# Performance work log

Measured on AMD Instinct MI355X. Metric: run time of the kernel, lower is better.

The kernel has to match this reference:

```python
import jax, jax.numpy as jnp
import numpy as np

N, E, H, C, HC = 16384, 262144, 4, 128, 512
G, IN, ED, OUT, NCLS = 8, 5, 2, 256, 12
EPS = 1e-5


def _gatv2(x, src, dst, ea, Wl, Wr, We, att, b):
    # GATv2Conv (PyG): score = att . leaky_relu(lin_l(x_j) + lin_r(x_i) + lin_e(e))
    xl = (x @ Wl).reshape(-1, H, C)          # source transform [N,H,C]
    xr = (x @ Wr).reshape(-1, H, C)          # target transform [N,H,C]
    ee = (ea @ We).reshape(-1, H, C)         # edge embedding   [E,H,C]
    s = jax.nn.leaky_relu(xl[src] + xr[dst] + ee, 0.2)
    logit = jnp.einsum('ehc,hc->eh', s, att)            # [E,H]
    m = jax.ops.segment_max(logit, dst, num_segments=N)  # per-dst max
    a = jnp.exp(logit - m[dst])
    denom = jax.ops.segment_sum(a, dst, num_segments=N)
    alpha = a / (denom[dst] + 1e-16)                     # segment softmax
    out = jax.ops.segment_sum(xl[src] * alpha[:, :, None], dst, num_segments=N)
    return out.reshape(-1, HC) + b


def _bn(x, g, b):  # BatchNorm1d, training-mode batch stats
    mu = x.mean(0)
    var = x.var(0)
    return g * (x - mu) * jax.lax.rsqrt(var + EPS) + b


def setup_inputs() -> dict:
    key = jax.random.key(0)
    ks = iter(jax.random.split(key, 32))
    d = {}
    d['x'] = jax.random.normal(next(ks), (N, IN), jnp.float32)
    d['edge_attr'] = jax.random.normal(next(ks), (E, ED), jnp.float32)
    d['edge_index'] = jax.random.randint(next(ks), (2, E), 0, N)
    d['batch'] = jnp.sort(jax.random.randint(next(ks), (N,), 0, G))
    for i, din in zip((1, 2, 3), (IN, HC, HC)):
        d[f'c{i}_Wl'] = jax.random.normal(next(ks), (din, HC), jnp.float32) * 0.05
        d[f'c{i}_Wr'] = jax.random.normal(next(ks), (din, HC), jnp.float32) * 0.05
        d[f'c{i}_We'] = jax.random.normal(next(ks), (ED, HC), jnp.float32) * 0.05
        d[f'c{i}_att'] = jax.random.normal(next(ks), (H, C), jnp.float32) * 0.05
        d[f'c{i}_b'] = jnp.zeros((HC,), jnp.float32)
        d[f'bn{i}_g'] = jnp.ones((HC,), jnp.float32)
        d[f'bn{i}_b'] = jnp.zeros((HC,), jnp.float32)
    d['ge_W1'] = jax.random.normal(next(ks), (HC, OUT), jnp.float32) * 0.05
    d['ge_b1'] = jnp.zeros((OUT,), jnp.float32)
    d['ge_W2'] = jax.random.normal(next(ks), (OUT, OUT), jnp.float32) * 0.05
    d['ge_b2'] = jnp.zeros((OUT,), jnp.float32)
    d['cls_W'] = jax.random.normal(next(ks), (OUT, NCLS), jnp.float32) * 0.05
    d['cls_b'] = jnp.zeros((NCLS,), jnp.float32)
    return d


def reference(x, edge_attr, edge_index, batch,
              c1_Wl, c1_Wr, c1_We, c1_att, c1_b, bn1_g, bn1_b,
              c2_Wl, c2_Wr, c2_We, c2_att, c2_b, bn2_g, bn2_b,
              c3_Wl, c3_Wr, c3_We, c3_att, c3_b, bn3_g, bn3_b,
              ge_W1, ge_b1, ge_W2, ge_b2, cls_W, cls_b):
    src, dst = edge_index[0], edge_index[1]
    x1 = jax.nn.elu(_bn(_gatv2(x, src, dst, edge_attr, c1_Wl, c1_Wr, c1_We, c1_att, c1_b), bn1_g, bn1_b))
    x2 = jax.nn.elu(_bn(_gatv2(x1, src, dst, edge_attr, c2_Wl, c2_Wr, c2_We, c2_att, c2_b), bn2_g, bn2_b)) + x1
    x3 = jax.nn.elu(_bn(_gatv2(x2, src, dst, edge_attr, c3_Wl, c3_Wr, c3_We, c3_att, c3_b), bn3_g, bn3_b)) + x2
    cnt = jax.ops.segment_sum(jnp.ones((N,), x3.dtype), batch, num_segments=G)
    x_pool = jax.ops.segment_sum(x3, batch, num_segments=G) / cnt[:, None]
    emb = jax.nn.relu(x_pool @ ge_W1 + ge_b1) @ ge_W2 + ge_b2
    logits = emb @ cls_W + cls_b
    return logits, emb
```

## Files before the change

kernel.cpp:

```cpp
#include <hip/hip_runtime.h>
#include <math.h>

#define NN    16384
#define NE    262144
#define NHEAD 4
#define HC    512
#define NG    8

typedef __bf16 bf16x8 __attribute__((ext_vector_type(8)));
typedef float floatx4 __attribute__((ext_vector_type(4)));
typedef float f32x2 __attribute__((ext_vector_type(2)));

__device__ __forceinline__ f32x2 sp2(float s) { return (f32x2){s, s}; }
__device__ __forceinline__ f32x2 pkmax(f32x2 a, f32x2 b) {
    f32x2 r; r.x = fmaxf(a.x, b.x); r.y = fmaxf(a.y, b.y); return r;
}

__device__ __forceinline__ unsigned short f2bf(float f) {
    union { float f; unsigned u; } v{f};
    unsigned r = v.u + 0x7FFFu + ((v.u >> 16) & 1u);
    return (unsigned short)(r >> 16);
}
__device__ __forceinline__ float bf2f(unsigned short b) {
    return __uint_as_float((unsigned)b << 16);
}

__device__ __forceinline__ void unpk8v(uint4 v, f32x2* f) {
    f[0] = (f32x2){__uint_as_float(v.x << 16), __uint_as_float(v.x & 0xFFFF0000u)};
    f[1] = (f32x2){__uint_as_float(v.y << 16), __uint_as_float(v.y & 0xFFFF0000u)};
    f[2] = (f32x2){__uint_as_float(v.z << 16), __uint_as_float(v.z & 0xFFFF0000u)};
    f[3] = (f32x2){__uint_as_float(v.w << 16), __uint_as_float(v.w & 0xFFFF0000u)};
}

#define GLD16(g, l) __builtin_amdgcn_global_load_lds( \
    (const __attribute__((address_space(1))) void*)(g), \
    (__attribute__((address_space(3))) void*)(l), 16, 0, 0)

__global__ __launch_bounds__(1024) void k_scan(const int* __restrict__ cnt,
                                               int* __restrict__ rp,
                                               int* __restrict__ offp,
                                               const int* __restrict__ batch,
                                               int* __restrict__ gcnt) {
    __shared__ int part[1024];
    int t = threadIdx.x;
    if (t < NG) {
        int lb[2];
#pragma unroll
        for (int q = 0; q < 2; q++) {
            int target = t + q;
            int lo = 0, hi = NN;
            while (lo < hi) {
                int mid = (lo + hi) >> 1;
                if (batch[mid] < target) lo = mid + 1; else hi = mid;
            }
            lb[q] = lo;
        }
        gcnt[t] = lb[1] - lb[0];
    }
    int base = t * 16;
    int loc[16];
    int s = 0;
#pragma unroll
    for (int i = 0; i < 16; i++) { loc[i] = s; s += cnt[base + i]; }
    part[t] = s;
    __syncthreads();
    for (int off = 1; off < 1024; off <<= 1) {
        int v = 0;
        if (t >= off) v = part[t - off];
        __syncthreads();
        if (t >= off) part[t] += v;
        __syncthreads();
    }
    int excl = (t == 0) ? 0 : part[t - 1];
#pragma unroll
    for (int i = 0; i < 16; i++) {
        int r = excl + loc[i];
        rp[base + i] = r;
        offp[base + i] = r;
    }
    if (t == 1023) rp[NN] = excl + s;
}

__global__ void k_fill(const int* __restrict__ dst, const int* __restrict__ src,
                       const float* __restrict__ ea, int* __restrict__ offp,
                       int* __restrict__ csrc, float2* __restrict__ ce) {
    int e = blockIdx.x * 256 + threadIdx.x;
    if (e < NE) {
        int d = dst[e];
        int pos = atomicAdd(&offp[d], 1);
        csrc[pos] = src[e];
        ce[pos] = *(const float2*)(ea + 2 * (size_t)e);
    }
}

__global__ __launch_bounds__(256) void k_pre(
        const int* __restrict__ dst, int* __restrict__ cnt,
        const float* __restrict__ W0, const float* __restrict__ W1,
        const float* __restrict__ W2, const float* __restrict__ W3,
        unsigned short* __restrict__ Wt2, unsigned short* __restrict__ Wt3,
        const float* __restrict__ x, const float* __restrict__ Wl,
        const float* __restrict__ Wr,
        unsigned short* __restrict__ xl, unsigned short* __restrict__ xr) {
    __shared__ float tile[64][65];
    int bid = blockIdx.x;
    int t = threadIdx.x;
    if (bid >= 1280) {
        int n = (bid - 1280) * 4 + (t >> 6);
        int lane = t & 63;
        int j0 = lane << 3;
        float xs[5];
#pragma unroll
        for (int k = 0; k < 5; k++) xs[k] = x[n * 5 + k];
        float al[8] = {}, ar[8] = {};
#pragma unroll
        for (int k = 0; k < 5; k++) {
            float4 wl0 = *(const float4*)(Wl + k * 512 + j0);
            float4 wl1 = *(const float4*)(Wl + k * 512 + j0 + 4);
            float4 wr0 = *(const float4*)(Wr + k * 512 + j0);
            float4 wr1 = *(const float4*)(Wr + k * 512 + j0 + 4);
            al[0] += xs[k] * wl0.x; al[1] += xs[k] * wl0.y; al[2] += xs[k] * wl0.z; al[3] += xs[k] * wl0.w;
            al[4] += xs[k] * wl1.x; al[5] += xs[k] * wl1.y; al[6] += xs[k] * wl1.z; al[7] += xs[k] * wl1.w;
            ar[0] += xs[k] * wr0.x; ar[1] += xs[k] * wr0.y; ar[2] += xs[k] * wr0.z; ar[3] += xs[k] * wr0.w;
            ar[4] += xs[k] * wr1.x; ar[5] += xs[k] * wr1.y; ar[6] += xs[k] * wr1.z; ar[7] += xs[k] * wr1.w;
        }
        ushort4 o0, o1;
        o0.x = f2bf(al[0]); o0.y = f2bf(al[1]); o0.z = f2bf(al[2]); o0.w = f2bf(al[3]);
        o1.x = f2bf(al[4]); o1.y = f2bf(al[5]); o1.z = f2bf(al[6]); o1.w = f2bf(al[7]);
        *(ushort4*)(xl + (size_t)n * 512 + j0) = o0;
        *(ushort4*)(xl + (size_t)n * 512 + j0 + 4) = o1;
        o0.x = f2bf(ar[0]); o0.y = f2bf(ar[1]); o0.z = f2bf(ar[2]); o0.w = f2bf(ar[3]);
        o1.x = f2bf(ar[4]); o1.y = f2bf(ar[5]); o1.z = f2bf(ar[6]); o1.w = f2bf(ar[7]);
        *(ushort4*)(xr + (size_t)n * 512 + j0) = o0;
        *(ushort4*)(xr + (size_t)n * 512 + j0 + 4) = o1;
    } else if (bid >= 1024) {
        int wb = bid - 1024;
        int mat = wb >> 6, sub = wb & 63;
        const float* W = (mat == 0) ? W0 : (mat == 1) ? W1 : (mat == 2) ? W2 : W3;
        unsigned short* Wt = (mat == 0) ? Wt2 : (mat == 1) ? (Wt2 + 512 * 512)
                           : (mat == 2) ? Wt3 : (Wt3 + 512 * 512);
        int n0 = (sub & 7) * 64, k0 = (sub >> 3) * 64;
        int lr = t >> 4;
        int lc = (t & 15) << 2;
        for (int r = lr; r < 64; r += 16) {
            float4 v = *(const float4*)(W + (size_t)(k0 + r) * 512 + n0 + lc);
            tile[r][lc] = v.x; tile[r][lc + 1] = v.y; tile[r][lc + 2] = v.z; tile[r][lc + 3] = v.w;
        }
        __syncthreads();
        for (int r = lr; r < 64; r += 16) {
            ushort4 o;
            o.x = f2bf(tile[lc + 0][r]); o.y = f2bf(tile[lc + 1][r]);
            o.z = f2bf(tile[lc + 2][r]); o.w = f2bf(tile[lc + 3][r]);
            *(ushort4*)(Wt + (size_t)(n0 + r) * 512 + k0 + lc) = o;
        }
    } else {
        int e = bid * 256 + t;
        atomicAdd(&cnt[dst[e]], 1);
    }
}

#define BM 128
#define BN 128
#define BK 64

__global__ __launch_bounds__(256) void k_gemm_bf16(
        const unsigned short* __restrict__ Ab,
        const unsigned short* __restrict__ Bt,
        unsigned short* __restrict__ xl, unsigned short* __restrict__ xr) {
    __shared__ unsigned short As[BM * BK];
    __shared__ unsigned short Bs[BN * BK];
    int t = threadIdx.x;
    int bid = blockIdx.x;
    int xcd = bid & 7, r = bid >> 3;
    int m0 = (xcd * 16 + (r & 15)) * BM;
    int n0 = (r >> 4) * BN;
    int wid = t >> 6, lane = t & 63;
    int wm = (wid >> 1) * 64, wn = (wid & 1) * 64;
    int lrow = lane & 15, quad = lane >> 4;
    floatx4 acc[4][4] = {};
    for (int k0 = 0; k0 < 512; k0 += BK) {
        __syncthreads();
#pragma unroll
        for (int it = 0; it < 4; it++) {
            int cid = it * 256 + t;
            int row = cid >> 3, ch = cid & 7;
            GLD16(Ab + (size_t)(m0 + row) * 512 + k0 + ch * 8, As + cid * 8);
            GLD16(Bt + (size_t)(n0 + row) * 512 + k0 + ch * 8, Bs + cid * 8);
        }
        __syncthreads();
#pragma unroll
        for (int ko = 0; ko < 2; ko++) {
            bf16x8 af[4], bfr[4];
#pragma unroll
            for (int i = 0; i < 4; i++) {
                af[i]  = *(const bf16x8*)&As[(wm + i * 16 + lrow) * BK + ko * 32 + quad * 8];
                bfr[i] = *(const bf16x8*)&Bs[(wn + i * 16 + lrow) * BK + ko * 32 + quad * 8];
            }
#pragma unroll
            for (int i = 0; i < 4; i++)
#pragma unroll
                for (int j = 0; j < 4; j++)
                    acc[i][j] = __builtin_amdgcn_mfma_f32_16x16x32_bf16(af[i], bfr[j], acc[i][j], 0, 0, 0);
        }
    }
#pragma unroll
    for (int i = 0; i < 4; i++) {
        int row = m0 + wm + i * 16 + quad * 4;
#pragma unroll
        for (int j = 0; j < 4; j++) {
            int col = n0 + wn + j * 16 + lrow;
            unsigned short* dstp = (col < 512) ? (xl + (size_t)row * 512 + col)
                                               : (xr + (size_t)row * 512 + (col - 512));
#pragma unroll
            for (int rr = 0; rr < 4; rr++) dstp[(size_t)rr * 512] = f2bf(acc[i][j][rr]);
        }
    }
}

__global__ __launch_bounds__(64) void k_attn(
        const unsigned short* __restrict__ xl, const unsigned short* __restrict__ xr,
        const int* __restrict__ rp, const int* __restrict__ csrc,
        const float2* __restrict__ ce, const float* __restrict__ We,
        const float* __restrict__ att, const float* __restrict__ bias,
        unsigned short* __restrict__ out) {
    int n = __builtin_amdgcn_readfirstlane(blockIdx.x);
    int lane = threadIdx.x;
    int c0 = lane << 3;
    f32x2 wv0[4], wv1[4], av[4], rv[4];
    {
        float4 a = *(const float4*)(We + c0), b = *(const float4*)(We + c0 + 4);
        wv0[0] = (f32x2){a.x, a.y}; wv0[1] = (f32x2){a.z, a.w};
        wv0[2] = (f32x2){b.x, b.y}; wv0[3] = (f32x2){b.z, b.w};
        a = *(const float4*)(We + 512 + c0); b = *(const float4*)(We + 512 + c0 + 4);
        wv1[0] = (f32x2){a.x, a.y}; wv1[1] = (f32x2){a.z, a.w};
        wv1[2] = (f32x2){b.x, b.y}; wv1[3] = (f32x2){b.z, b.w};
        a = *(const float4*)(att + c0); b = *(const float4*)(att + c0 + 4);
        av[0] = (f32x2){a.x, a.y}; av[1] = (f32x2){a.z, a.w};
        av[2] = (f32x2){b.x, b.y}; av[3] = (f32x2){b.z, b.w};
        uint4 vr = *(const uint4*)(xr + (size_t)n * 512 + c0);
        unpk8v(vr, rv);
    }
    float l = 0.f;
    f32x2 acc[4] = {sp2(0.f), sp2(0.f), sp2(0.f), sp2(0.f)};
    int beg = rp[n], end = rp[n + 1];
    uint4 cv[4];
    float2 cev[4];
    if (beg < end) {
#pragma unroll
        for (int k = 0; k < 4; k++) {
            int q = beg + k; q = (q < end) ? q : end - 1;
            cv[k] = *(const uint4*)(xl + (size_t)csrc[q] * 512 + c0);
            cev[k] = ce[q];
        }
    }
    int i = beg;
    for (; i + 3 < end; i += 4) {
        uint4 a[4]; float2 d[4];
#pragma unroll
        for (int k = 0; k < 4; k++) { a[k] = cv[k]; d[k] = cev[k]; }
#pragma unroll
        for (int k = 0; k < 4; k++) {
            int q = i + 4 + k; q = (q < end) ? q : end - 1;
            cv[k] = *(const uint4*)(xl + (size_t)csrc[q] * 512 + c0);
            cev[k] = ce[q];
        }
        f32x2 lv[4][4];
#pragma unroll
        for (int k = 0; k < 4; k++) unpk8v(a[k], lv[k]);
        float p[4];
#pragma unroll
        for (int k = 0; k < 4; k++) {
            f32x2 dx = sp2(d[k].x), dy = sp2(d[k].y);
            f32x2 pv = sp2(0.f);
#pragma unroll
            for (int j = 0; j < 4; j++) {
                f32x2 v = lv[k][j] + rv[j] + dx * wv0[j] + dy * wv1[j];
                v = pkmax(v, sp2(0.2f) * v);
                pv += av[j] * v;
            }
            p[k] = pv.x + pv.y;
        }
#pragma unroll
        for (int m = 1; m <= 8; m <<= 1) {
#pragma unroll
            for (int k = 0; k < 4; k++) p[k] += __shfl_xor(p[k], m);
        }
        float w[4];
#pragma unroll
        for (int k = 0; k < 4; k++) { w[k] = __expf(fminf(p[k], 60.f)); l += w[k]; }
#pragma unroll
        for (int j = 0; j < 4; j++) {
            f32x2 t0 = sp2(w[0]) * lv[0][j] + sp2(w[1]) * lv[1][j];
            f32x2 t1 = sp2(w[2]) * lv[2][j] + sp2(w[3]) * lv[3][j];
            acc[j] += t0 + t1;
        }
    }
    int rem = end - i;
#pragma unroll
    for (int k = 0; k < 3; k++) {
        if (k < rem) {
            f32x2 lv[4];
            unpk8v(cv[k], lv);
            f32x2 dx = sp2(cev[k].x), dy = sp2(cev[k].y);
            f32x2 pv = sp2(0.f);
#pragma unroll
            for (int j = 0; j < 4; j++) {
                f32x2 v = lv[j] + rv[j] + dx * wv0[j] + dy * wv1[j];
                v = pkmax(v, sp2(0.2f) * v);
                pv += av[j] * v;
            }
            float p = pv.x + pv.y;
            p += __shfl_xor(p, 1);
            p += __shfl_xor(p, 2);
            p += __shfl_xor(p, 4);
            p += __shfl_xor(p, 8);
            float w = __expf(fminf(p, 60.f));
            l += w;
            f32x2 wv = sp2(w);
#pragma unroll
            for (int j = 0; j < 4; j++) acc[j] += wv * lv[j];
        }
    }
    float inv = 1.f / (l + 1e-16f);
    const float* bb = bias + c0;
    float4 b0 = *(const float4*)bb, b1 = *(const float4*)(bb + 4);
    ushort4 o0, o1;
    o0.x = f2bf(acc[0].x * inv + b0.x); o0.y = f2bf(acc[0].y * inv + b0.y);
    o0.z = f2bf(acc[1].x * inv + b0.z); o0.w = f2bf(acc[1].y * inv + b0.w);
    o1.x = f2bf(acc[2].x * inv + b1.x); o1.y = f2bf(acc[2].y * inv + b1.y);
    o1.z = f2bf(acc[3].x * inv + b1.z); o1.w = f2bf(acc[3].y * inv + b1.w);
    *(ushort4*)(out + (size_t)n * 512 + c0) = o0;
    *(ushort4*)(out + (size_t)n * 512 + c0 + 4) = o1;
}

__global__ __launch_bounds__(256) void k_bnstat(const unsigned short* __restrict__ xb,
                                                double* __restrict__ sum,
                                                double* __restrict__ sumsq) {
    __shared__ float ls[4][512];
    __shared__ float lq[4][512];
    int t = threadIdx.x;
    int w = t >> 6, lane = t & 63;
    int c0 = lane << 3;
    int r0 = blockIdx.x * 64 + w * 16;
    f32x2 sv[4] = {sp2(0.f), sp2(0.f), sp2(0.f), sp2(0.f)};
    f32x2 qv[4] = {sp2(0.f), sp2(0.f), sp2(0.f), sp2(0.f)};
#pragma unroll 4
    for (int r = r0; r < r0 + 16; r++) {
        uint4 u = *(const uint4*)(xb + (size_t)r * 512 + c0);
        f32x2 v[4];
        unpk8v(u, v);
#pragma unroll
        for (int j = 0; j < 4; j++) { sv[j] += v[j]; qv[j] += v[j] * v[j]; }
    }
#pragma unroll
    for (int j = 0; j < 4; j++) {
        ls[w][c0 + 2 * j] = sv[j].x; ls[w][c0 + 2 * j + 1] = sv[j].y;
        lq[w][c0 + 2 * j] = qv[j].x; lq[w][c0 + 2 * j + 1] = qv[j].y;
    }
    __syncthreads();
    int c2 = t << 1;
#pragma unroll
    for (int k = 0; k < 2; k++) {
        int c = c2 + k;
        float s4 = ls[0][c] + ls[1][c] + ls[2][c] + ls[3][c];
        float q4 = lq[0][c] + lq[1][c] + lq[2][c] + lq[3][c];
        atomicAdd(sum + c, (double)s4);
        atomicAdd(sumsq + c, (double)q4);
    }
}

__global__ void k_bnapply(const unsigned short* __restrict__ v,
                          const unsigned short* __restrict__ resid,
                          const double* __restrict__ sum, const double* __restrict__ sumsq,
                          const float* __restrict__ g, const float* __restrict__ beta,
                          unsigned short* __restrict__ outb) {
    int i = (blockIdx.x * 256 + threadIdx.x) << 2;
    int c = i & 511;
    ushort4 vu = *(const ushort4*)(v + i);
    double2 s01 = *(const double2*)(sum + c);
    double2 s23 = *(const double2*)(sum + c + 2);
    double2 q01 = *(const double2*)(sumsq + c);
    double2 q23 = *(const double2*)(sumsq + c + 2);
    float4 gg = *(const float4*)(g + c);
    float4 be = *(const float4*)(beta + c);
    const double invN = 1.0 / NN;
    double mu0 = s01.x * invN, mu1 = s01.y * invN, mu2 = s23.x * invN, mu3 = s23.y * invN;
    float sc0 = gg.x * rsqrtf((float)(q01.x * invN - mu0 * mu0) + 1e-5f);
    float sc1 = gg.y * rsqrtf((float)(q01.y * invN - mu1 * mu1) + 1e-5f);
    float sc2 = gg.z * rsqrtf((float)(q23.x * invN - mu2 * mu2) + 1e-5f);
    float sc3 = gg.w * rsqrtf((float)(q23.y * invN - mu3 * mu3) + 1e-5f);
    float y0 = (bf2f(vu.x) - (float)mu0) * sc0 + be.x;
    float y1 = (bf2f(vu.y) - (float)mu1) * sc1 + be.y;
    float y2 = (bf2f(vu.z) - (float)mu2) * sc2 + be.z;
    float y3 = (bf2f(vu.w) - (float)mu3) * sc3 + be.w;
    y0 = y0 > 0.f ? y0 : expm1f(y0);
    y1 = y1 > 0.f ? y1 : expm1f(y1);
    y2 = y2 > 0.f ? y2 : expm1f(y2);
    y3 = y3 > 0.f ? y3 : expm1f(y3);
    if (resid) {
        ushort4 ru = *(const ushort4*)(resid + i);
        y0 += bf2f(ru.x); y1 += bf2f(ru.y); y2 += bf2f(ru.z); y3 += bf2f(ru.w);
    }
    ushort4 o;
    o.x = f2bf(y0); o.y = f2bf(y1); o.z = f2bf(y2); o.w = f2bf(y3);
    *(ushort4*)(outb + i) = o;
}

__global__ __launch_bounds__(256) void k_pool(const unsigned short* __restrict__ xb,
                                              const int* __restrict__ batch,
                                              float* __restrict__ pooled) {
    __shared__ float lacc[NG][512];
    int t = threadIdx.x;
    for (int i = t; i < NG * 512; i += 256) ((float*)lacc)[i] = 0.f;
    __syncthreads();
    int r0 = blockIdx.x * 64;
    int c2 = t << 1;
    for (int r = r0; r < r0 + 64; r++) {
        int g = batch[r];
        unsigned u = *(const unsigned*)(xb + (size_t)r * 512 + c2);
        lacc[g][c2]     += __uint_as_float(u << 16);
        lacc[g][c2 + 1] += __uint_as_float(u & 0xFFFF0000u);
    }
    __syncthreads();
    int gmin = batch[r0], gmax = batch[r0 + 63];
    for (int g = gmin; g <= gmax; g++)
        for (int i = t; i < 512; i += 256)
            atomicAdd(&pooled[g * 512 + i], lacc[g][i]);
}

__global__ __launch_bounds__(256) void k_head_h1(const float* __restrict__ pooled,
                                                 const float* __restrict__ W1,
                                                 float* __restrict__ h1acc) {
    int g = blockIdx.x >> 4, s = blockIdx.x & 15;
    int o = threadIdx.x;
    int c0 = s * 32;
    float acc = 0.f;
#pragma unroll
    for (int c = 0; c < 32; c++)
        acc += pooled[g * 512 + c0 + c] * W1[(size_t)(c0 + c) * 256 + o];
    atomicAdd(&h1acc[g * 256 + o], acc);
}

__global__ __launch_bounds__(256) void k_head_emb(const float* __restrict__ h1acc,
                                                  const int* __restrict__ gcnt,
                                                  const float* __restrict__ b1,
                                                  const float* __restrict__ W2,
                                                  float* __restrict__ embacc) {
    __shared__ float hs[32];
    int g = blockIdx.x >> 3, s = blockIdx.x & 7;
    int c0 = s * 32;
    int t = threadIdx.x;
    if (t < 32) {
        float inv = 1.f / (float)gcnt[g];
        hs[t] = fmaxf(h1acc[g * 256 + c0 + t] * inv + b1[c0 + t], 0.f);
    }
    __syncthreads();
    float acc = 0.f;
#pragma unroll
    for (int c = 0; c < 32; c++)
        acc += hs[c] * W2[(size_t)(c0 + c) * 256 + t];
    atomicAdd(&embacc[g * 256 + t], acc);
}

__global__ __launch_bounds__(256) void k_head_fin(const float* __restrict__ embacc,
                                                  const float* __restrict__ b2,
                                                  const float* __restrict__ clsW,
                                                  const float* __restrict__ clsb,
                                                  float* __restrict__ outp) {
    __shared__ float es[256];
    int g = blockIdx.x, o = threadIdx.x;
    float e = embacc[g * 256 + o] + b2[o];
    outp[NG * 12 + g * 256 + o] = e;
    es[o] = e;
    __syncthreads();
    if (o < 12) {
        float lg = clsb[o];
        for (int c = 0; c < 256; c++) lg += es[c] * clsW[c * 12 + o];
        outp[g * 12 + o] = lg;
    }
}

extern "C" void kernel_launch(void* const* d_in, const int* in_sizes, int n_in,
                              void* d_out, int out_size, void* d_ws, size_t ws_size,
                              hipStream_t stream) {
    const float* x     = (const float*)d_in[0];
    const float* ea    = (const float*)d_in[1];
    const int*   ei    = (const int*)d_in[2];
    const int*   batch = (const int*)d_in[3];
    const int* src = ei;
    const int* dst = ei + NE;

    float* base = (float*)d_ws;
    size_t off = 0;
    auto alloc = [&](size_t n) -> float* {
        float* p = base + off;
        off += (n + 255) & ~(size_t)255;
        return p;
    };
    unsigned short* xl  = (unsigned short*)alloc((size_t)NN * 256);
    unsigned short* xr  = (unsigned short*)alloc((size_t)NN * 256);
    unsigned short* Yb  = (unsigned short*)alloc((size_t)NN * 256);
    unsigned short* XbA = (unsigned short*)alloc((size_t)NN * 256);
    unsigned short* XbB = (unsigned short*)alloc((size_t)NN * 256);
    unsigned short* Wt2 = (unsigned short*)alloc(512 * 1024 / 2);
    unsigned short* Wt3 = (unsigned short*)alloc(512 * 1024 / 2);
    int*      rp    = (int*)alloc(NN + 1);
    int*      offp  = (int*)alloc(NN);
    int*      csrc  = (int*)alloc(NE);
    float2*   ce    = (float2*)alloc((size_t)NE * 2);
    int*      cnt   = (int*)alloc(NN);
    double*   bsum3 = (double*)alloc(3 * 2048);
    float*    pooled= alloc(NG * 512);
    float*    h1acc = alloc(NG * 256);
    float*    embacc= alloc(NG * 256);
    int*      gcnt  = (int*)alloc(NG);
    float*    outp  = (float*)d_out;

    hipMemsetAsync(cnt, 0, 30720 * sizeof(float), stream);
    k_pre<<<5376, 256, 0, stream>>>(dst, cnt,
                                    (const float*)d_in[11], (const float*)d_in[12],
                                    (const float*)d_in[18], (const float*)d_in[19],
                                    Wt2, Wt3,
                                    x, (const float*)d_in[4], (const float*)d_in[5],
                                    xl, xr);
    k_scan<<<1, 1024, 0, stream>>>(cnt, rp, offp, batch, gcnt);
    k_fill<<<NE / 256, 256, 0, stream>>>(dst, src, ea, offp, csrc, ce);

    unsigned short* X = XbA;
    unsigned short* Xp = XbB;
    for (int l = 0; l < 3; l++) {
        const float* We  = (const float*)d_in[4 + l * 7 + 2];
        const float* att = (const float*)d_in[4 + l * 7 + 3];
        const float* cb  = (const float*)d_in[4 + l * 7 + 4];
        const float* bg  = (const float*)d_in[4 + l * 7 + 5];
        const float* bb  = (const float*)d_in[4 + l * 7 + 6];

        if (l > 0) {
            k_gemm_bf16<<<1024, 256, 0, stream>>>(Xp, (l == 1) ? Wt2 : Wt3, xl, xr);
        }
        k_attn<<<NN, 64, 0, stream>>>(xl, xr, rp, csrc, ce, We, att, cb, Yb);

        double* bsum = bsum3 + l * 1024;
        double* bsq  = bsum + 512;
        k_bnstat<<<256, 256, 0, stream>>>(Yb, bsum, bsq);
        k_bnapply<<<(size_t)NN * 512 / 1024, 256, 0, stream>>>(
            Yb, (l == 0) ? nullptr : Xp, bsum, bsq, bg, bb, X);

        unsigned short* tmp = Xp; Xp = X; X = tmp;
    }

    k_pool<<<NN / 64, 256, 0, stream>>>(Xp, batch, pooled);

    const float* geW1 = (const float*)d_in[25];
    const float* geb1 = (const float*)d_in[26];
    const float* geW2 = (const float*)d_in[27];
    const float* geb2 = (const float*)d_in[28];
    const float* clsW = (const float*)d_in[29];
    const float* clsb = (const float*)d_in[30];

    k_head_h1<<<NG * 16, 256, 0, stream>>>(pooled, geW1, h1acc);
    k_head_emb<<<NG * 8, 256, 0, stream>>>(h1acc, gcnt, geb1, geW2, embacc);
    k_head_fin<<<NG, 256, 0, stream>>>(embacc, geb2, clsW, clsb, outp);
}
```

Before: 463.2 us.

## Fuse BN stat/apply and pooling/head kernels via cooperative grid sync

Merges the BatchNorm statistics and apply kernels into one cooperative kernel that uses a grid-wide sync between the reduction and the normalize/ELU/residual pass. Each block now handles 8 chunks in the apply phase and computes the per-channel scale once. It also fuses pooling and the three head MLP kernels into one cooperative kernel with grid syncs between stages. The aim is to cut kernel launch overheads and tail gaps. The cost is that grid sync and cooperative launch need all 1024 blocks to be co-resident, and grid barriers are not free.

```diff
diff --git a/kernel.cpp b/kernel.cpp
--- a/kernel.cpp
+++ b/kernel.cpp
@@ -1,5 +1,8 @@
 #include <hip/hip_runtime.h>
+#include <hip/hip_cooperative_groups.h>
 #include <math.h>
+
+namespace cg = cooperative_groups;
 
 #define NN    16384
 #define NE    262144
@@ -332,50 +335,49 @@
     *(ushort4*)(out + (size_t)n * 512 + c0 + 4) = o1;
 }
 
-__global__ __launch_bounds__(256) void k_bnstat(const unsigned short* __restrict__ xb,
-                                                double* __restrict__ sum,
-                                                double* __restrict__ sumsq) {
+__global__ __launch_bounds__(256) void k_bn(
+        const unsigned short* __restrict__ v,
+        const unsigned short* __restrict__ resid,
+        double* __restrict__ sum, double* __restrict__ sumsq,
+        const float* __restrict__ g, const float* __restrict__ beta,
+        unsigned short* __restrict__ outb) {
+    cg::grid_group gridg = cg::this_grid();
     __shared__ float ls[4][512];
     __shared__ float lq[4][512];
     int t = threadIdx.x;
-    int w = t >> 6, lane = t & 63;
-    int c0 = lane << 3;
-    int r0 = blockIdx.x * 64 + w * 16;
-    f32x2 sv[4] = {sp2(0.f), sp2(0.f), sp2(0.f), sp2(0.f)};
-    f32x2 qv[4] = {sp2(0.f), sp2(0.f), sp2(0.f), sp2(0.f)};
+    int bid = blockIdx.x;
+    if (bid < 256) {
+        int w = t >> 6, lane = t & 63;
+        int c0 = lane << 3;
+        int r0 = bid * 64 + w * 16;
+        f32x2 sv[4] = {sp2(0.f), sp2(0.f), sp2(0.f), sp2(0.f)};
+        f32x2 qv[4] = {sp2(0.f), sp2(0.f), sp2(0.f), sp2(0.f)};
 #pragma unroll 4
-    for (int r = r0; r < r0 + 16; r++) {
-        uint4 u = *(const uint4*)(xb + (size_t)r * 512 + c0);
-        f32x2 v[4];
-        unpk8v(u, v);
-#pragma unroll
-        for (int j = 0; j < 4; j++) { sv[j] += v[j]; qv[j] += v[j] * v[j]; }
-    }
-#pragma unroll
-    for (int j = 0; j < 4; j++) {
-        ls[w][c0 + 2 * j] = sv[j].x; ls[w][c0 + 2 * j + 1] = sv[j].y;
-        lq[w][c0 + 2 * j] = qv[j].x; lq[w][c0 + 2 * j + 1] = qv[j].y;
-    }
-    __syncthreads();
-    int c2 = t << 1;
-#pragma unroll
-    for (int k = 0; k < 2; k++) {
-        int c = c2 + k;
-        float s4 = ls[0][c] + ls[1][c] + ls[2][c] + ls[3][c];
-        float q4 = lq[0][c] + lq[1][c] + lq[2][c] + lq[3][c];
-        atomicAdd(sum + c, (double)s4);
-        atomicAdd(sumsq + c, (double)q4);
-    }
-}
-
-__global__ void k_bnapply(const unsigned short* __restrict__ v,
-                          const unsigned short* __restrict__ resid,
-                          const double* __restrict__ sum, const double* __restrict__ sumsq,
-                          const float* __restrict__ g, const float* __restrict__ beta,
-                          unsigned short* __restrict__ outb) {
-    int i = (blockIdx.x * 256 + threadIdx.x) << 2;
-    int c = i & 511;
-    ushort4 vu = *(const ushort4*)(v + i);
+        for (int r = r0; r < r0 + 16; r++) {
+            uint4 u = *(const uint4*)(v + (size_t)r * 512 + c0);
+            f32x2 vv[4];
+            unpk8v(u, vv);
+#pragma unroll
+            for (int j = 0; j < 4; j++) { sv[j] += vv[j]; qv[j] += vv[j] * vv[j]; }
+        }
+#pragma unroll
+        for (int j = 0; j < 4; j++) {
+            ls[w][c0 + 2 * j] = sv[j].x; ls[w][c0 + 2 * j + 1] = sv[j].y;
+            lq[w][c0 + 2 * j] = qv[j].x; lq[w][c0 + 2 * j + 1] = qv[j].y;
+        }
+        __syncthreads();
+        int c2 = t << 1;
+#pragma unroll
+        for (int k = 0; k < 2; k++) {
+            int c = c2 + k;
+            float s4 = ls[0][c] + ls[1][c] + ls[2][c] + ls[3][c];
+            float q4 = lq[0][c] + lq[1][c] + lq[2][c] + lq[3][c];
+            atomicAdd(sum + c, (double)s4);
+            atomicAdd(sumsq + c, (double)q4);
+        }
+    }
+    gridg.sync();
+    int c = (t << 2) & 511;
     double2 s01 = *(const double2*)(sum + c);
     double2 s23 = *(const double2*)(sum + c + 2);
     double2 q01 = *(const double2*)(sumsq + c);
@@ -388,94 +390,97 @@
     float sc1 = gg.y * rsqrtf((float)(q01.y * invN - mu1 * mu1) + 1e-5f);
     float sc2 = gg.z * rsqrtf((float)(q23.x * invN - mu2 * mu2) + 1e-5f);
     float sc3 = gg.w * rsqrtf((float)(q23.y * invN - mu3 * mu3) + 1e-5f);
-    float y0 = (bf2f(vu.x) - (float)mu0) * sc0 + be.x;
-    float y1 = (bf2f(vu.y) - (float)mu1) * sc1 + be.y;
-    float y2 = (bf2f(vu.z) - (float)mu2) * sc2 + be.z;
-    float y3 = (bf2f(vu.w) - (float)mu3) * sc3 + be.w;
-    y0 = y0 > 0.f ? y0 : expm1f(y0);
-    y1 = y1 > 0.f ? y1 : expm1f(y1);
-    y2 = y2 > 0.f ? y2 : expm1f(y2);
-    y3 = y3 > 0.f ? y3 : expm1f(y3);
-    if (resid) {
-        ushort4 ru = *(const ushort4*)(resid + i);
-        y0 += bf2f(ru.x); y1 += bf2f(ru.y); y2 += bf2f(ru.z); y3 += bf2f(ru.w);
-    }
-    ushort4 o;
-    o.x = f2bf(y0); o.y = f2bf(y1); o.z = f2bf(y2); o.w = f2bf(y3);
-    *(ushort4*)(outb + i) = o;
-}
-
-__global__ __launch_bounds__(256) void k_pool(const unsigned short* __restrict__ xb,
-                                              const int* __restrict__ batch,
-                                              float* __restrict__ pooled) {
+    float fm0 = (float)mu0, fm1 = (float)mu1, fm2 = (float)mu2, fm3 = (float)mu3;
+#pragma unroll
+    for (int q = 0; q < 8; q++) {
+        int i = (((bid << 3) | q) * 256 + t) << 2;
+        ushort4 vu = *(const ushort4*)(v + i);
+        float y0 = (bf2f(vu.x) - fm0) * sc0 + be.x;
+        float y1 = (bf2f(vu.y) - fm1) * sc1 + be.y;
+        float y2 = (bf2f(vu.z) - fm2) * sc2 + be.z;
+        float y3 = (bf2f(vu.w) - fm3) * sc3 + be.w;
+        y0 = y0 > 0.f ? y0 : expm1f(y0);
+        y1 = y1 > 0.f ? y1 : expm1f(y1);
+        y2 = y2 > 0.f ? y2 : expm1f(y2);
+        y3 = y3 > 0.f ? y3 : expm1f(y3);
+        if (resid) {
+            ushort4 ru = *(const ushort4*)(resid + i);
+            y0 += bf2f(ru.x); y1 += bf2f(ru.y); y2 += bf2f(ru.z); y3 += bf2f(ru.w);
+        }
+        ushort4 o;
+        o.x = f2bf(y0); o.y = f2bf(y1); o.z = f2bf(y2); o.w = f2bf(y3);
+        *(ushort4*)(outb + i) = o;
+    }
+}
+
+__global__ __launch_bounds__(256) void k_head_all(
+        const unsigned short* __restrict__ xb, const int* __restrict__ batch,
+        float* __restrict__ pooled, const int* __restrict__ gcnt,
+        const float* __restrict__ W1, const float* __restrict__ b1,
+        const float* __restrict__ W2, const float* __restrict__ b2,
+        const float* __restrict__ clsW, const float* __restrict__ clsb,
+        float* __restrict__ h1acc, float* __restrict__ embacc,
+        float* __restrict__ outp) {
+    cg::grid_group gridg = cg::this_grid();
     __shared__ float lacc[NG][512];
     int t = threadIdx.x;
+    int bid = blockIdx.x;
     for (int i = t; i < NG * 512; i += 256) ((float*)lacc)[i] = 0.f;
     __syncthreads();
-    int r0 = blockIdx.x * 64;
-    int c2 = t << 1;
-    for (int r = r0; r < r0 + 64; r++) {
-        int g = batch[r];
-        unsigned u = *(const unsigned*)(xb + (size_t)r * 512 + c2);
-        lacc[g][c2]     += __uint_as_float(u << 16);
-        lacc[g][c2 + 1] += __uint_as_float(u & 0xFFFF0000u);
-    }
-    __syncthreads();
-    int gmin = batch[r0], gmax = batch[r0 + 63];
-    for (int g = gmin; g <= gmax; g++)
-        for (int i = t; i < 512; i += 256)
-            atomicAdd(&pooled[g * 512 + i], lacc[g][i]);
-}
-
-__global__ __launch_bounds__(256) void k_head_h1(const float* __restrict__ pooled,
-                                                 const float* __restrict__ W1,
-                                                 float* __restrict__ h1acc) {
-    int g = blockIdx.x >> 4, s = blockIdx.x & 15;
-    int o = threadIdx.x;
-    int c0 = s * 32;
-    float acc = 0.f;
-#pragma unroll
-    for (int c = 0; c < 32; c++)
-        acc += pooled[g * 512 + c0 + c] * W1[(size_t)(c0 + c) * 256 + o];
-    atomicAdd(&h1acc[g * 256 + o], acc);
-}
-
-__global__ __launch_bounds__(256) void k_head_emb(const float* __restrict__ h1acc,
-                                                  const int* __restrict__ gcnt,
-                                                  const float* __restrict__ b1,
-                                                  const float* __restrict__ W2,
-                                                  float* __restrict__ embacc) {
-    __shared__ float hs[32];
-    int g = blockIdx.x >> 3, s = blockIdx.x & 7;
-    int c0 = s * 32;
-    int t = threadIdx.x;
-    if (t < 32) {
-        float inv = 1.f / (float)gcnt[g];
-        hs[t] = fmaxf(h1acc[g * 256 + c0 + t] * inv + b1[c0 + t], 0.f);
-    }
-    __syncthreads();
-    float acc = 0.f;
-#pragma unroll
-    for (int c = 0; c < 32; c++)
-        acc += hs[c] * W2[(size_t)(c0 + c) * 256 + t];
-    atomicAdd(&embacc[g * 256 + t], acc);
-}
-
-__global__ __launch_bounds__(256) void k_head_fin(const float* __restrict__ embacc,
-                                                  const float* __restrict__ b2,
-                                                  const float* __restrict__ clsW,
-                                                  const float* __restrict__ clsb,
-                                                  float* __restrict__ outp) {
-    __shared__ float es[256];
-    int g = blockIdx.x, o = threadIdx.x;
-    float e = embacc[g * 256 + o] + b2[o];
-    outp[NG * 12 + g * 256 + o] = e;
-    es[o] = e;
-    __syncthreads();
-    if (o < 12) {
-        float lg = clsb[o];
-        for (int c = 0; c < 256; c++) lg += es[c] * clsW[c * 12 + o];
-        outp[g * 12 + o] = lg;
+    {
+        int r0 = bid * 64;
+        int c2 = t << 1;
+        for (int r = r0; r < r0 + 64; r++) {
+            int g = batch[r];
+            unsigned u = *(const unsigned*)(xb + (size_t)r * 512 + c2);
+            lacc[g][c2]     += __uint_as_float(u << 16);
+            lacc[g][c2 + 1] += __uint_as_float(u & 0xFFFF0000u);
+        }
+        __syncthreads();
+        int gmin = batch[r0], gmax = batch[r0 + 63];
+        for (int g = gmin; g <= gmax; g++)
+            for (int i = t; i < 512; i += 256)
+                atomicAdd(&pooled[g * 512 + i], lacc[g][i]);
+    }
+    gridg.sync();
+    if (bid < 128) {
+        int g = bid >> 4, s = bid & 15;
+        int c0 = s * 32;
+        float acc = 0.f;
+#pragma unroll
+        for (int c = 0; c < 32; c++)
+            acc += pooled[g * 512 + c0 + c] * W1[(size_t)(c0 + c) * 256 + t];
+        atomicAdd(&h1acc[g * 256 + t], acc);
+    }
+    gridg.sync();
+    if (bid < 64) {
+        int g = bid >> 3, s = bid & 7;
+        int c0 = s * 32;
+        float* hs = &lacc[0][0];
+        if (t < 32) {
+            float inv = 1.f / (float)gcnt[g];
+            hs[t] = fmaxf(h1acc[g * 256 + c0 + t] * inv + b1[c0 + t], 0.f);
+        }
+        __syncthreads();
+        float acc = 0.f;
+#pragma unroll
+        for (int c = 0; c < 32; c++)
+            acc += hs[c] * W2[(size_t)(c0 + c) * 256 + t];
+        atomicAdd(&embacc[g * 256 + t], acc);
+    }
+    gridg.sync();
+    if (bid < 8) {
+        int g = bid;
+        float* es = &lacc[1][0];
+        float e = embacc[g * 256 + t] + b2[t];
+        outp[NG * 12 + g * 256 + t] = e;
+        es[t] = e;
+        __syncthreads();
+        if (t < 12) {
+            float lg = clsb[t];
+            for (int c = 0; c < 256; c++) lg += es[c] * clsW[c * 12 + t];
+            outp[g * 12 + t] = lg;
+        }
     }
 }
 
@@ -541,14 +546,16 @@
 
         double* bsum = bsum3 + l * 1024;
         double* bsq  = bsum + 512;
-        k_bnstat<<<256, 256, 0, stream>>>(Yb, bsum, bsq);
-        k_bnapply<<<(size_t)NN * 512 / 1024, 256, 0, stream>>>(
-            Yb, (l == 0) ? nullptr : Xp, bsum, bsq, bg, bb, X);
+        const unsigned short* vin = Yb;
+        const unsigned short* residp = (l == 0) ? nullptr : (const unsigned short*)Xp;
+        unsigned short* outbp = X;
+        void* bnArgs[] = {(void*)&vin, (void*)&residp, (void*)&bsum, (void*)&bsq,
+                          (void*)&bg, (void*)&bb, (void*)&outbp};
+        hipLaunchCooperativeKernel((const void*)k_bn, dim3(1024), dim3(256),
+                                   bnArgs, 0, stream);
 
         unsigned short* tmp = Xp; Xp = X; X = tmp;
     }
-
-    k_pool<<<NN / 64, 256, 0, stream>>>(Xp, batch, pooled);
 
     const float* geW1 = (const float*)d_in[25];
     const float* geb1 = (const float*)d_in[26];
@@ -557,7 +564,11 @@
     const float* clsW = (const float*)d_in[29];
     const float* clsb = (const float*)d_in[30];
 
-    k_head_h1<<<NG * 16, 256, 0, stream>>>(pooled, geW1, h1acc);
-    k_head_emb<<<NG * 8, 256, 0, stream>>>(h1acc, gcnt, geb1, geW2, embacc);
-    k_head_fin<<<NG, 256, 0, stream>>>(embacc, geb2, clsW, clsb, outp);
-}
+    const unsigned short* xbin = (const unsigned short*)Xp;
+    void* headArgs[] = {(void*)&xbin, (void*)&batch, (void*)&pooled, (void*)&gcnt,
+                        (void*)&geW1, (void*)&geb1, (void*)&geW2, (void*)&geb2,
+                        (void*)&clsW, (void*)&clsb, (void*)&h1acc, (void*)&embacc,
+                        (void*)&outp};
+    hipLaunchCooperativeKernel((const void*)k_head_all, dim3(256), dim3(256),
+                               headArgs, 0, stream);
+}
```

New measurement: 814.7 us. +75.9%, slower.
